# Kernel tuning notes

Measured on AMD Instinct MI355X. Metric: run time of the kernel, lower is better.

## Reference

```python
import jax, jax.numpy as jnp
import numpy as np

B, T, D, H = 1024, 200, 64, 64


def setup_inputs() -> dict:
    key = jax.random.key(0)
    ks = jax.random.split(key, 24)
    s = 0.05
    inp = {
        'dense_inputs': jax.random.normal(ks[0], (B, 4), jnp.float32),
        'sparse_inputs': jax.random.randint(ks[1], (B, 2), 0, 1000),
        'seq_inputs': jax.random.randint(ks[2], (B, T, 1), 0, 1000000),
        'item_inputs': jax.random.randint(ks[3], (B, 1), 0, 1000000),
        'hist_len': jax.random.randint(ks[4], (B,), 1, T + 1),
        'item_table': jax.random.normal(ks[5], (1000000, D), jnp.float32) * s,
        'other_tables': jax.random.normal(ks[6], (2, 1000, 16), jnp.float32) * s,
        'gru_W': jax.random.normal(ks[7], (D, 3 * H), jnp.float32) * s,
        'gru_U': jax.random.normal(ks[8], (H, 3 * H), jnp.float32) * s,
        'gru_b': jnp.zeros((3 * H,), jnp.float32),
        'aug_W': jax.random.normal(ks[9], (H, 3 * H), jnp.float32) * s,
        'aug_U': jax.random.normal(ks[10], (H, 3 * H), jnp.float32) * s,
        'aug_b': jnp.zeros((3 * H,), jnp.float32),
        'att_W1': jax.random.normal(ks[11], (4 * D, 64), jnp.float32) * s,
        'att_b1': jnp.zeros((64,), jnp.float32),
        'att_W2': jax.random.normal(ks[12], (64, 16), jnp.float32) * s,
        'att_b2': jnp.zeros((16,), jnp.float32),
        'att_W3': jax.random.normal(ks[13], (16, 1), jnp.float32) * s,
        'att_b3': jnp.zeros((1,), jnp.float32),
        'ffn_W1': jax.random.normal(ks[14], (164, 256), jnp.float32) * s,
        'ffn_b1': jnp.zeros((256,), jnp.float32),
        'ffn_W2': jax.random.normal(ks[15], (256, 128), jnp.float32) * s,
        'ffn_b2': jnp.zeros((128,), jnp.float32),
        'ffn_W3': jax.random.normal(ks[16], (128, 64), jnp.float32) * s,
        'ffn_b3': jnp.zeros((64,), jnp.float32),
        'out_W': jax.random.normal(ks[17], (64, 1), jnp.float32) * s,
        'out_b': jnp.zeros((1,), jnp.float32),
    }
    return inp


def _gru_scan(x_tbd, valid_tb, W, U, b, att_tb=None):
    """Masked (AU)GRU scan. x_tbd: [T,B,D]; valid_tb: [T,B] bool; att_tb: [T,B] or None.
    Returns (final_state [B,H], seq_states [T,B,H])."""
    h0 = jnp.zeros((x_tbd.shape[1], H), x_tbd.dtype)

    def step(h, inp):
        x, valid, a = inp
        xw = x @ W + b            # [B,3H]
        hu = h @ U                # [B,3H]
        z = jax.nn.sigmoid(xw[:, :H] + hu[:, :H])
        r = jax.nn.sigmoid(xw[:, H:2 * H] + hu[:, H:2 * H])
        hh = jnp.tanh(xw[:, 2 * H:] + r * hu[:, 2 * H:])
        if a is not None:
            z = a[:, None] * z    # AUGRU: attention-scaled update gate
        h_new = (1.0 - z) * h + z * hh
        h = jnp.where(valid[:, None], h_new, h)
        return h, h

    xs = (x_tbd, valid_tb, att_tb)
    if att_tb is None:
        def step2(h, inp):
            return step(h, (inp[0], inp[1], None))
        return jax.lax.scan(step2, h0, (x_tbd, valid_tb))
    return jax.lax.scan(step, h0, xs)


def _dice(x):
    # Dice activation at alpha=0: p=sigmoid(batch-standardized x); out = p*x
    m = jnp.mean(x, axis=0, keepdims=True)
    v = jnp.var(x, axis=0, keepdims=True)
    p = jax.nn.sigmoid((x - m) * jax.lax.rsqrt(v + 1e-9))
    return p * x


def reference(dense_inputs, sparse_inputs, seq_inputs, item_inputs, hist_len,
              item_table, other_tables, gru_W, gru_U, gru_b, aug_W, aug_U, aug_b,
              att_W1, att_b1, att_W2, att_b2, att_W3, att_b3,
              ffn_W1, ffn_b1, ffn_W2, ffn_b2, ffn_W3, ffn_b3, out_W, out_b):
    # Embedding lookups
    seq_embed = item_table[seq_inputs[:, :, 0]]          # [B,T,D]
    target_embed = item_table[item_inputs[:, 0]]         # [B,D]
    other = jnp.concatenate([other_tables[i][sparse_inputs[:, i]] for i in range(2)], axis=-1)  # [B,32]
    other_info = jnp.concatenate([dense_inputs, other], axis=-1)  # [B,36]

    valid_tb = jnp.arange(T)[:, None] < hist_len[None, :]  # [T,B]

    # Interest extraction: plain GRU over behavior sequence
    _, seq_h_tbh = _gru_scan(jnp.transpose(seq_embed, (1, 0, 2)), valid_tb, gru_W, gru_U, gru_b)
    seq_h = jnp.transpose(seq_h_tbh, (1, 0, 2))           # [B,T,H]

    # DIN-style target attention: MLP over [q, k, q-k, q*k]
    qt = jnp.broadcast_to(target_embed[:, None, :], seq_h.shape)
    feats = jnp.concatenate([qt, seq_h, qt - seq_h, qt * seq_h], axis=-1)  # [B,T,4D]
    prelu = lambda x: jnp.where(x > 0, x, 0.25 * x)
    a = prelu(feats @ att_W1 + att_b1)
    a = prelu(a @ att_W2 + att_b2)
    logits = (a @ att_W3 + att_b3)[..., 0]                # [B,T]
    logits = jnp.where(valid_tb.T, logits, -1e9)
    scores = jax.nn.softmax(logits, axis=-1)              # [B,T]

    # Interest evolution: AUGRU gated by attention scores
    final_state, _ = _gru_scan(seq_h_tbh, valid_tb, aug_W, aug_U, aug_b, att_tb=scores.T)

    out = jnp.concatenate([final_state, target_embed, other_info], axis=-1)  # [B,164]
    out = _dice(out @ ffn_W1 + ffn_b1)
    out = _dice(out @ ffn_W2 + ffn_b2)
    out = _dice(out @ ffn_W3 + ffn_b3)
    out = jax.nn.sigmoid(out @ out_W + out_b)             # [B,1]
    return out
```

## Files before the change

### kernel.cpp

```cpp
#include <hip/hip_runtime.h>

#define BB 1024
#define TT 200

typedef __attribute__((ext_vector_type(8))) short short8;
typedef __attribute__((ext_vector_type(4))) float f32x4;

__device__ __forceinline__ float sigmoidf_(float x) { return __fdividef(1.0f, 1.0f + __expf(-x)); }
__device__ __forceinline__ float tanh_fast(float x) {
    x = fminf(15.f, fmaxf(-15.f, x));
    float e = __expf(-2.f * x);
    return __fdividef(1.f - e, 1.f + e);
}
__device__ __forceinline__ float dicef_(float x, float m, float v) {
    return x * sigmoidf_((x - m) * rsqrtf(v + 1e-9f));
}
__device__ __forceinline__ unsigned short f2bf(float f) {
    unsigned u = __float_as_uint(f);
    unsigned r = u + 0x7fffu + ((u >> 16) & 1u);
    return (unsigned short)(r >> 16);
}
__device__ __forceinline__ float bf2f(unsigned short h) {
    return __uint_as_float(((unsigned)h) << 16);
}
__device__ __forceinline__ unsigned cvt_pk_bf16(float lo, float hi) {
    unsigned r;
    asm("v_cvt_pk_bf16_f32 %0, %1, %2" : "=v"(r) : "v"(lo), "v"(hi));
    return r;
}
union U8 { short8 s8; unsigned u[4]; };

__global__ void k_prep(const float* __restrict__ dense, const int* __restrict__ sparse,
                       const int* __restrict__ item_idx, const float* __restrict__ table,
                       const float* __restrict__ other_tables,
                       float* __restrict__ target, float* __restrict__ other) {
    int b = blockIdx.x, l = threadIdx.x;
    target[b * 64 + l] = table[(size_t)item_idx[b] * 64 + l];
    if (l < 4) other[b * 36 + l] = dense[b * 4 + l];
    else if (l < 20) other[b * 36 + l] = other_tables[(size_t)sparse[b * 2 + 0] * 16 + (l - 4)];
    else if (l < 36) other[b * 36 + l] = other_tables[1000 * 16 + (size_t)sparse[b * 2 + 1] * 16 + (l - 20)];
}

template <int GATHER>
__global__ __launch_bounds__(256, 1) void k_xw(
    const int* __restrict__ idx, const float* __restrict__ tablef,
    const unsigned short* __restrict__ Abf,
    const float* __restrict__ W, const float* __restrict__ bias,
    unsigned short* __restrict__ out, int Mtiles, int tilestride)
{
    const int l = threadIdx.x & 63;
    const int wv = threadIdx.x >> 6;
    const int lg = l >> 4;
    const int li = l & 15;

    short8 bfr[12][2];
    float bn[12];
#pragma unroll
    for (int nt = 0; nt < 12; ++nt) {
        bn[nt] = bias[nt * 16 + li];
#pragma unroll
        for (int c = 0; c < 2; ++c) {
#pragma unroll
            for (int j = 0; j < 8; ++j) {
                int k = c * 32 + lg * 8 + j;
                bfr[nt][c][j] = (short)f2bf(W[k * 192 + nt * 16 + li]);
            }
        }
    }

    for (int tile = blockIdx.x * 4 + wv; tile < Mtiles; tile += tilestride) {
        short8 a[2];
        if (GATHER) {
            long row = (long)tile * 16 + li;
            long id = idx[row];
            const float* tp = tablef + id * 64 + lg * 8;
#pragma unroll
            for (int c = 0; c < 2; ++c) {
                f32x4 v0 = *(const f32x4*)(tp + c * 32);
                f32x4 v1 = *(const f32x4*)(tp + c * 32 + 4);
#pragma unroll
                for (int j = 0; j < 4; ++j) {
                    a[c][j] = (short)f2bf(v0[j]);
                    a[c][4 + j] = (short)f2bf(v1[j]);
                }
            }
        } else {
            long row = (long)tile * 16 + li;
#pragma unroll
            for (int c = 0; c < 2; ++c)
                a[c] = *(const short8*)(Abf + row * 64 + c * 32 + lg * 8);
        }

        f32x4 acc[12];
#pragma unroll
        for (int nt = 0; nt < 12; ++nt) acc[nt] = (f32x4){0.f, 0.f, 0.f, 0.f};
#pragma unroll
        for (int c = 0; c < 2; ++c)
#pragma unroll
            for (int nt = 0; nt < 12; ++nt)
                acc[nt] = __builtin_amdgcn_mfma_f32_16x16x32_bf16(a[c], bfr[nt][c], acc[nt], 0, 0, 0);

#pragma unroll
        for (int nt = 0; nt < 12; ++nt)
#pragma unroll
            for (int j = 0; j < 4; ++j) {
                long row = (long)tile * 16 + lg * 4 + j;
                out[row * 192 + nt * 16 + li] = f2bf(acc[nt][j] + bn[nt]);
            }
    }
}

template <int AUG>
__global__ __launch_bounds__(256, 1) void k_scan2(
    const unsigned short* __restrict__ xw,
    const float* __restrict__ U,
    const int* __restrict__ hist_len,
    const float* __restrict__ scores,
    unsigned short* __restrict__ hout,
    float* __restrict__ hfinal)
{
    __shared__ float h_lds[4][64];
    const int w = threadIdx.x >> 6, l = threadIdx.x & 63;
    const int b = blockIdx.x * 4 + w;

    float Uz[64], Ur[64], Uh[64];
#pragma unroll
    for (int k = 0; k < 64; ++k) {
        Uz[k] = U[k * 192 + l];
        Ur[k] = U[k * 192 + 64 + l];
        Uh[k] = U[k * 192 + 128 + l];
    }
    const int mylen = hist_len[b];
    const unsigned short* xwr = xw + (size_t)b * TT * 192;
    const float* scr = scores + (size_t)b * TT;
    unsigned short* hor = hout + (size_t)b * TT * 64;

    float h = 0.f;
    h_lds[w][l] = 0.f;
    asm volatile("" ::: "memory");

    unsigned short nz = xwr[l], nr = xwr[64 + l], nh = xwr[128 + l];
    float ns = AUG ? scr[0] : 0.f;

    for (int t = 0; t < TT; ++t) {
        const unsigned short cz = nz, cr = nr, ch = nh;
        const float cs = ns;
        if (t + 1 < TT) {
            const unsigned short* p = xwr + (size_t)(t + 1) * 192;
            nz = p[l]; nr = p[64 + l]; nh = p[128 + l];
            if (AUG) ns = scr[t + 1];
        }

        float az = 0.f, ar = 0.f, ah = 0.f;
        const float4* h4 = (const float4*)(&h_lds[w][0]);
#pragma unroll
        for (int kc = 0; kc < 16; ++kc) {
            float4 hv = h4[kc];
            az += hv.x * Uz[4*kc] + hv.y * Uz[4*kc+1] + hv.z * Uz[4*kc+2] + hv.w * Uz[4*kc+3];
            ar += hv.x * Ur[4*kc] + hv.y * Ur[4*kc+1] + hv.z * Ur[4*kc+2] + hv.w * Ur[4*kc+3];
            ah += hv.x * Uh[4*kc] + hv.y * Uh[4*kc+1] + hv.z * Uh[4*kc+2] + hv.w * Uh[4*kc+3];
        }

        float zg = sigmoidf_(bf2f(cz) + az);
        float rg = sigmoidf_(bf2f(cr) + ar);
        float hh = tanh_fast(bf2f(ch) + rg * ah);
        if (AUG) zg *= cs;
        float hn = (1.f - zg) * h + zg * hh;
        h = (t < mylen) ? hn : h;

        asm volatile("" ::: "memory");
        h_lds[w][l] = h;
        asm volatile("" ::: "memory");
        if (!AUG) hor[(size_t)t * 64 + l] = f2bf(h);
    }
    if (AUG) hfinal[(size_t)b * 64 + l] = h;
}

__global__ __launch_bounds__(256, 2) void k_att(
    const float* __restrict__ target, const unsigned short* __restrict__ seq_hb,
    const float* __restrict__ W1, const float* __restrict__ b1,
    const float* __restrict__ W2, const float* __restrict__ b2,
    const float* __restrict__ W3, const float* __restrict__ b3,
    const int* __restrict__ hist_len, float* __restrict__ scores)
{
    __shared__ unsigned short W1f[8 * 4 * 64 * 8];
    __shared__ float a1s[4][16][68];
    __shared__ float logit_lds[208];
    __shared__ float red[8];

    const int tid = threadIdx.x;
    const int wv = tid >> 6, l = tid & 63;
    const int lg = l >> 4, li = l & 15;
    const int b = blockIdx.x;
    const int len = hist_len[b];

    for (int i = tid; i < 8 * 4 * 64 * 8; i += 256) {
        int j = i & 7, ll = (i >> 3) & 63, nt = (i >> 9) & 3, c = i >> 11;
        int k = c * 32 + (ll >> 4) * 8 + j;
        int col = nt * 16 + (ll & 15);
        W1f[i] = f2bf(W1[k * 64 + col]);
    }
    __syncthreads();

    short8 w1r[8][4];
    const short8* wf = (const short8*)W1f;
#pragma unroll
    for (int c = 0; c < 8; ++c)
#pragma unroll
        for (int nt = 0; nt < 4; ++nt)
            w1r[c][nt] = wf[(c * 4 + nt) * 64 + l];

    short8 w2r[2];
#pragma unroll
    for (int c = 0; c < 2; ++c) {
        U8 t8;
#pragma unroll
        for (int m = 0; m < 4; ++m) {
            int k0 = c * 32 + lg * 8 + 2 * m;
            t8.u[m] = cvt_pk_bf16(W2[k0 * 16 + li], W2[(k0 + 1) * 16 + li]);
        }
        w2r[c] = t8.s8;
    }

    float b1v[4];
#pragma unroll
    for (int nt = 0; nt < 4; ++nt) b1v[nt] = b1[nt * 16 + li];
    const float b2v = b2[li];
    const float w3v = W3[li];
    const float b3r = b3[0];

    const float* qp = target + (size_t)b * 64;
    float qf_lo[8], qf_hi[8];
#pragma unroll
    for (int j = 0; j < 8; ++j) { qf_lo[j] = qp[lg * 8 + j]; qf_hi[j] = qp[32 + lg * 8 + j]; }
    U8 q8l, q8h;
#pragma unroll
    for (int m = 0; m < 4; ++m) {
        q8l.u[m] = cvt_pk_bf16(qf_lo[2 * m], qf_lo[2 * m + 1]);
        q8h.u[m] = cvt_pk_bf16(qf_hi[2 * m], qf_hi[2 * m + 1]);
    }

    for (int mt = wv; mt < 13; mt += 4) {
        const int t = mt * 16 + li;
        const int tld = (t < TT) ? t : TT - 1;
        const unsigned short* hp = seq_hb + ((size_t)b * TT + tld) * 64 + lg * 8;
        short8 h8l = *(const short8*)hp;
        short8 h8h = *(const short8*)(hp + 32);

        float hf;
        U8 d8l, d8h, m8l, m8h;
#pragma unroll
        for (int m = 0; m < 4; ++m) {
            float h0, h1, d0, d1, p0, p1;
            h0 = bf2f((unsigned short)h8l[2 * m]); h1 = bf2f((unsigned short)h8l[2 * m + 1]);
            d0 = qf_lo[2 * m] - h0; d1 = qf_lo[2 * m + 1] - h1;
            p0 = qf_lo[2 * m] * h0; p1 = qf_lo[2 * m + 1] * h1;
            d8l.u[m] = cvt_pk_bf16(d0, d1);
            m8l.u[m] = cvt_pk_bf16(p0, p1);
            h0 = bf2f((unsigned short)h8h[2 * m]); h1 = bf2f((unsigned short)h8h[2 * m + 1]);
            d0 = qf_hi[2 * m] - h0; d1 = qf_hi[2 * m + 1] - h1;
            p0 = qf_hi[2 * m] * h0; p1 = qf_hi[2 * m + 1] * h1;
            d8h.u[m] = cvt_pk_bf16(d0, d1);
            m8h.u[m] = cvt_pk_bf16(p0, p1);
        }
        (void)hf;

        f32x4 acc[4];
#pragma unroll
        for (int nt = 0; nt < 4; ++nt) acc[nt] = (f32x4){0.f, 0.f, 0.f, 0.f};
#pragma unroll
        for (int nt = 0; nt < 4; ++nt) {
            acc[nt] = __builtin_amdgcn_mfma_f32_16x16x32_bf16(q8l.s8, w1r[0][nt], acc[nt], 0, 0, 0);
            acc[nt] = __builtin_amdgcn_mfma_f32_16x16x32_bf16(q8h.s8, w1r[1][nt], acc[nt], 0, 0, 0);
            acc[nt] = __builtin_amdgcn_mfma_f32_16x16x32_bf16(h8l,    w1r[2][nt], acc[nt], 0, 0, 0);
            acc[nt] = __builtin_amdgcn_mfma_f32_16x16x32_bf16(h8h,    w1r[3][nt], acc[nt], 0, 0, 0);
            acc[nt] = __builtin_amdgcn_mfma_f32_16x16x32_bf16(d8l.s8, w1r[4][nt], acc[nt], 0, 0, 0);
            acc[nt] = __builtin_amdgcn_mfma_f32_16x16x32_bf16(d8h.s8, w1r[5][nt], acc[nt], 0, 0, 0);
            acc[nt] = __builtin_amdgcn_mfma_f32_16x16x32_bf16(m8l.s8, w1r[6][nt], acc[nt], 0, 0, 0);
            acc[nt] = __builtin_amdgcn_mfma_f32_16x16x32_bf16(m8h.s8, w1r[7][nt], acc[nt], 0, 0, 0);
        }

#pragma unroll
        for (int nt = 0; nt < 4; ++nt)
#pragma unroll
            for (int jj = 0; jj < 4; ++jj) {
                float v = acc[nt][jj] + b1v[nt];
                a1s[wv][lg * 4 + jj][nt * 16 + li] = (v > 0.f) ? v : 0.25f * v;
            }

        const float* arow = &a1s[wv][li][0];
        f32x4 acc2 = (f32x4){0.f, 0.f, 0.f, 0.f};
#pragma unroll
        for (int c2 = 0; c2 < 2; ++c2) {
            f32x4 v0 = *(const f32x4*)(arow + c2 * 32 + lg * 8);
            f32x4 v1 = *(const f32x4*)(arow + c2 * 32 + lg * 8 + 4);
            U8 a2f;
            a2f.u[0] = cvt_pk_bf16(v0[0], v0[1]);
            a2f.u[1] = cvt_pk_bf16(v0[2], v0[3]);
            a2f.u[2] = cvt_pk_bf16(v1[0], v1[1]);
            a2f.u[3] = cvt_pk_bf16(v1[2], v1[3]);
            acc2 = __builtin_amdgcn_mfma_f32_16x16x32_bf16(a2f.s8, w2r[c2], acc2, 0, 0, 0);
        }

#pragma unroll
        for (int jj = 0; jj < 4; ++jj) {
            float a2 = acc2[jj] + b2v;
            a2 = (a2 > 0.f) ? a2 : 0.25f * a2;
            float part = a2 * w3v;
            part += __shfl_xor(part, 1);
            part += __shfl_xor(part, 2);
            part += __shfl_xor(part, 4);
            part += __shfl_xor(part, 8);
            int tt = mt * 16 + lg * 4 + jj;
            if (li == 0 && tt < TT)
                logit_lds[tt] = (tt < len) ? (part + b3r) : -1e9f;
        }
    }
    __syncthreads();

    float v = (tid < TT) ? logit_lds[tid] : -1e30f;
    float m = v;
#pragma unroll
    for (int s = 1; s < 64; s <<= 1) m = fmaxf(m, __shfl_xor(m, s));
    if (l == 0) red[wv] = m;
    __syncthreads();
    m = fmaxf(fmaxf(red[0], red[1]), fmaxf(red[2], red[3]));
    float e = (tid < TT) ? __expf(v - m) : 0.f;
    float sum = e;
#pragma unroll
    for (int s = 1; s < 64; s <<= 1) sum += __shfl_xor(sum, s);
    if (l == 0) red[4 + wv] = sum;
    __syncthreads();
    float inv = __fdividef(1.f, red[4] + red[5] + red[6] + red[7]);
    if (tid < TT) scores[(size_t)b * TT + tid] = e * inv;
}

__global__ __launch_bounds__(256) void k_fc1(const float* __restrict__ fin,
                                             const float* __restrict__ tgt,
                                             const float* __restrict__ oth,
                                             const float* __restrict__ Wt,
                                             const float* __restrict__ bvec,
                                             float* __restrict__ fout) {
    __shared__ float z0[164];
    int b = blockIdx.x, tid = threadIdx.x;
    if (tid < 64) z0[tid] = fin[b * 64 + tid];
    else if (tid < 128) z0[tid] = tgt[b * 64 + tid - 64];
    else if (tid < 164) z0[tid] = oth[b * 36 + tid - 128];
    __syncthreads();
    float acc = bvec[tid];
#pragma unroll 4
    for (int k = 0; k < 164; ++k) acc += z0[k] * Wt[k * 256 + tid];
    fout[(size_t)b * 256 + tid] = acc;
}

template <int F>
__global__ __launch_bounds__(256) void k_stats(const float* __restrict__ x, float* __restrict__ stat) {
    int c = blockIdx.x, tid = threadIdx.x;
    float s = 0.f, sq = 0.f;
    for (int i = tid; i < BB; i += 256) {
        float v = x[(size_t)i * F + c];
        s += v; sq += v * v;
    }
#pragma unroll
    for (int m = 1; m < 64; m <<= 1) { s += __shfl_xor(s, m); sq += __shfl_xor(sq, m); }
    __shared__ float rs[4], rq[4];
    if ((tid & 63) == 0) { rs[tid >> 6] = s; rq[tid >> 6] = sq; }
    __syncthreads();
    if (tid == 0) {
        float S = rs[0] + rs[1] + rs[2] + rs[3];
        float Q = rq[0] + rq[1] + rq[2] + rq[3];
        float mean = S * (1.f / BB);
        float var = Q * (1.f / BB) - mean * mean;
        stat[c] = mean;
        stat[F + c] = var;
    }
}

__global__ __launch_bounds__(256) void k_fc2(const float* __restrict__ f1,
                                             const float* __restrict__ st1,
                                             const float* __restrict__ Wt,
                                             const float* __restrict__ bvec,
                                             float* __restrict__ f2) {
    __shared__ float z[256];
    int b = blockIdx.x, tid = threadIdx.x;
    float x = f1[(size_t)b * 256 + tid];
    z[tid] = dicef_(x, st1[tid], st1[256 + tid]);
    __syncthreads();
    if (tid < 128) {
        float acc = bvec[tid];
#pragma unroll 4
        for (int k = 0; k < 256; ++k) acc += z[k] * Wt[k * 128 + tid];
        f2[(size_t)b * 128 + tid] = acc;
    }
}

__global__ __launch_bounds__(128) void k_fc3(const float* __restrict__ f2,
                                             const float* __restrict__ st2,
                                             const float* __restrict__ Wt,
                                             const float* __restrict__ bvec,
                                             float* __restrict__ f3) {
    __shared__ float z[128];
    int b = blockIdx.x, tid = threadIdx.x;
    float x = f2[(size_t)b * 128 + tid];
    z[tid] = dicef_(x, st2[tid], st2[128 + tid]);
    __syncthreads();
    if (tid < 64) {
        float acc = bvec[tid];
#pragma unroll 4
        for (int k = 0; k < 128; ++k) acc += z[k] * Wt[k * 64 + tid];
        f3[(size_t)b * 64 + tid] = acc;
    }
}

__global__ void k_out(const float* __restrict__ f3, const float* __restrict__ st3,
                      const float* __restrict__ outW, const float* __restrict__ outb,
                      float* __restrict__ out) {
    int b = blockIdx.x, l = threadIdx.x;
    float x = f3[(size_t)b * 64 + l];
    float z = dicef_(x, st3[l], st3[64 + l]);
    float p = z * outW[l];
#pragma unroll
    for (int m = 1; m < 64; m <<= 1) p += __shfl_xor(p, m);
    if (l == 0) out[b] = sigmoidf_(p + outb[0]);
}

extern "C" void kernel_launch(void* const* d_in, const int* in_sizes, int n_in,
                              void* d_out, int out_size, void* d_ws, size_t ws_size,
                              hipStream_t stream) {
    const float* dense      = (const float*)d_in[0];
    const int*   sparse     = (const int*)d_in[1];
    const int*   seq_idx    = (const int*)d_in[2];
    const int*   item_idx   = (const int*)d_in[3];
    const int*   hist_len   = (const int*)d_in[4];
    const float* item_table = (const float*)d_in[5];
    const float* other_tab  = (const float*)d_in[6];
    const float* gru_W = (const float*)d_in[7];
    const float* gru_U = (const float*)d_in[8];
    const float* gru_b = (const float*)d_in[9];
    const float* aug_W = (const float*)d_in[10];
    const float* aug_U = (const float*)d_in[11];
    const float* aug_b = (const float*)d_in[12];
    const float* att_W1 = (const float*)d_in[13];
    const float* att_b1 = (const float*)d_in[14];
    const float* att_W2 = (const float*)d_in[15];
    const float* att_b2 = (const float*)d_in[16];
    const float* att_W3 = (const float*)d_in[17];
    const float* att_b3 = (const float*)d_in[18];
    const float* ffn_W1 = (const float*)d_in[19];
    const float* ffn_b1 = (const float*)d_in[20];
    const float* ffn_W2 = (const float*)d_in[21];
    const float* ffn_b2 = (const float*)d_in[22];
    const float* ffn_W3 = (const float*)d_in[23];
    const float* ffn_b3 = (const float*)d_in[24];
    const float* out_W  = (const float*)d_in[25];
    const float* out_b  = (const float*)d_in[26];

    float* wsf = (float*)d_ws;
    unsigned short* xwb   = (unsigned short*)(wsf);
    unsigned short* seqhb = (unsigned short*)(wsf + 19660800);
    float* scores = wsf + 26214400;
    float* target = wsf + 26419200;
    float* other  = wsf + 26484736;
    float* finals = wsf + 26521600;
    float* f1     = wsf + 26587136;
    float* f2     = wsf + 26849280;
    float* f3     = wsf + 26980352;
    float* st1    = wsf + 27045888;
    float* st2    = wsf + 27046400;
    float* st3    = wsf + 27046656;

    float* dout = (float*)d_out;
    const int Mtiles = (BB * TT) / 16;

    k_prep<<<BB, 64, 0, stream>>>(dense, sparse, item_idx, item_table, other_tab, target, other);

    k_xw<1><<<800, 256, 0, stream>>>(seq_idx, item_table, nullptr, gru_W, gru_b, xwb, Mtiles, 3200);

    k_scan2<0><<<BB / 4, 256, 0, stream>>>(xwb, gru_U, hist_len, scores, seqhb, finals);

    k_att<<<BB, 256, 0, stream>>>(target, seqhb, att_W1, att_b1, att_W2, att_b2,
                                  att_W3, att_b3, hist_len, scores);

    k_xw<0><<<800, 256, 0, stream>>>(nullptr, nullptr, seqhb, aug_W, aug_b, xwb, Mtiles, 3200);

    k_scan2<1><<<BB / 4, 256, 0, stream>>>(xwb, aug_U, hist_len, scores, seqhb, finals);

    k_fc1<<<BB, 256, 0, stream>>>(finals, target, other, ffn_W1, ffn_b1, f1);
    k_stats<256><<<256, 256, 0, stream>>>(f1, st1);
    k_fc2<<<BB, 256, 0, stream>>>(f1, st1, ffn_W2, ffn_b2, f2);
    k_stats<128><<<128, 256, 0, stream>>>(f2, st2);
    k_fc3<<<BB, 128, 0, stream>>>(f2, st2, ffn_W3, ffn_b3, f3);
    k_stats<64><<<64, 256, 0, stream>>>(f3, st3);
    k_out<<<BB, 64, 0, stream>>>(f3, st3, out_W, out_b, dout);
}
```

Baseline: 479.7 us.

## Split GRU recurrence matvec across four waves per batch row with LDS reduction

The scan kernel now assigns one block per batch row instead of one wave per row, with each of four waves holding a 16-row slice of U. The waves compute partial gate dot products, reduce them through shared memory, and one wave, rotating by timestep, applies the gate nonlinearity and updates h. This cuts the serial per-step dot-product length and the register pressure, allowing higher occupancy and four times more blocks. In exchange it adds two block barriers and an LDS reduction on every timestep of the sequential chain.

```diff
diff --git a/kernel.cpp b/kernel.cpp
--- a/kernel.cpp
+++ b/kernel.cpp
@@ -111,7 +111,7 @@
 }
 
 template <int AUG>
-__global__ __launch_bounds__(256, 1) void k_scan2(
+__global__ __launch_bounds__(256, 4) void k_scan3(
     const unsigned short* __restrict__ xw,
     const float* __restrict__ U,
     const int* __restrict__ hist_len,
@@ -119,61 +119,74 @@
     unsigned short* __restrict__ hout,
     float* __restrict__ hfinal)
 {
-    __shared__ float h_lds[4][64];
-    const int w = threadIdx.x >> 6, l = threadIdx.x & 63;
-    const int b = blockIdx.x * 4 + w;
-
-    float Uz[64], Ur[64], Uh[64];
-#pragma unroll
-    for (int k = 0; k < 64; ++k) {
-        Uz[k] = U[k * 192 + l];
-        Ur[k] = U[k * 192 + 64 + l];
-        Uh[k] = U[k * 192 + 128 + l];
-    }
-    const int mylen = hist_len[b];
+    __shared__ float h_lds[64];
+    __shared__ float part[3][4][64];
+
+    const int tid = threadIdx.x;
+    const int w = tid >> 6, l = tid & 63;
+    const int b = blockIdx.x;
+
+    float Uz[16], Ur[16], Uh[16];
+#pragma unroll
+    for (int kk = 0; kk < 16; ++kk) {
+        int k = w * 16 + kk;
+        Uz[kk] = U[k * 192 + l];
+        Ur[kk] = U[k * 192 + 64 + l];
+        Uh[kk] = U[k * 192 + 128 + l];
+    }
     const unsigned short* xwr = xw + (size_t)b * TT * 192;
     const float* scr = scores + (size_t)b * TT;
     unsigned short* hor = hout + (size_t)b * TT * 64;
-
-    float h = 0.f;
-    h_lds[w][l] = 0.f;
-    asm volatile("" ::: "memory");
-
-    unsigned short nz = xwr[l], nr = xwr[64 + l], nh = xwr[128 + l];
-    float ns = AUG ? scr[0] : 0.f;
+    const int mylen = hist_len[b];
+
+    unsigned short nz = 0, nr_ = 0, nh = 0;
+    float ns = 0.f;
+    if (w == 0) {
+        nz = xwr[l]; nr_ = xwr[64 + l]; nh = xwr[128 + l];
+        if (AUG) ns = scr[0];
+        h_lds[l] = 0.f;
+    }
+    __syncthreads();
 
     for (int t = 0; t < TT; ++t) {
-        const unsigned short cz = nz, cr = nr, ch = nh;
-        const float cs = ns;
-        if (t + 1 < TT) {
+        if (t + 1 < TT && ((t + 1) & 3) == w) {
             const unsigned short* p = xwr + (size_t)(t + 1) * 192;
-            nz = p[l]; nr = p[64 + l]; nh = p[128 + l];
+            nz = p[l]; nr_ = p[64 + l]; nh = p[128 + l];
             if (AUG) ns = scr[t + 1];
         }
 
         float az = 0.f, ar = 0.f, ah = 0.f;
-        const float4* h4 = (const float4*)(&h_lds[w][0]);
-#pragma unroll
-        for (int kc = 0; kc < 16; ++kc) {
+        const float4* h4 = (const float4*)(&h_lds[w * 16]);
+#pragma unroll
+        for (int kc = 0; kc < 4; ++kc) {
             float4 hv = h4[kc];
             az += hv.x * Uz[4*kc] + hv.y * Uz[4*kc+1] + hv.z * Uz[4*kc+2] + hv.w * Uz[4*kc+3];
             ar += hv.x * Ur[4*kc] + hv.y * Ur[4*kc+1] + hv.z * Ur[4*kc+2] + hv.w * Ur[4*kc+3];
             ah += hv.x * Uh[4*kc] + hv.y * Uh[4*kc+1] + hv.z * Uh[4*kc+2] + hv.w * Uh[4*kc+3];
         }
-
-        float zg = sigmoidf_(bf2f(cz) + az);
-        float rg = sigmoidf_(bf2f(cr) + ar);
-        float hh = tanh_fast(bf2f(ch) + rg * ah);
-        if (AUG) zg *= cs;
-        float hn = (1.f - zg) * h + zg * hh;
-        h = (t < mylen) ? hn : h;
-
-        asm volatile("" ::: "memory");
-        h_lds[w][l] = h;
-        asm volatile("" ::: "memory");
-        if (!AUG) hor[(size_t)t * 64 + l] = f2bf(h);
-    }
-    if (AUG) hfinal[(size_t)b * 64 + l] = h;
+        part[0][w][l] = az;
+        part[1][w][l] = ar;
+        part[2][w][l] = ah;
+        __syncthreads();
+
+        if ((t & 3) == w) {
+            float azf = part[0][0][l] + part[0][1][l] + part[0][2][l] + part[0][3][l];
+            float arf = part[1][0][l] + part[1][1][l] + part[1][2][l] + part[1][3][l];
+            float ahf = part[2][0][l] + part[2][1][l] + part[2][2][l] + part[2][3][l];
+            float hprev = h_lds[l];
+
+            float zg = sigmoidf_(bf2f(nz) + azf);
+            float rg = sigmoidf_(bf2f(nr_) + arf);
+            float hh = tanh_fast(bf2f(nh) + rg * ahf);
+            if (AUG) zg *= ns;
+            float hn = (1.f - zg) * hprev + zg * hh;
+            float hval = (t < mylen) ? hn : hprev;
+            h_lds[l] = hval;
+            if (!AUG) hor[(size_t)t * 64 + l] = f2bf(hval);
+        }
+        __syncthreads();
+    }
+    if (AUG && w == 0) hfinal[(size_t)b * 64 + l] = h_lds[l];
 }
 
 __global__ __launch_bounds__(256, 2) void k_att(
@@ -247,7 +260,6 @@
         short8 h8l = *(const short8*)hp;
         short8 h8h = *(const short8*)(hp + 32);
 
-        float hf;
         U8 d8l, d8h, m8l, m8h;
 #pragma unroll
         for (int m = 0; m < 4; ++m) {
@@ -263,7 +275,6 @@
             d8h.u[m] = cvt_pk_bf16(d0, d1);
             m8h.u[m] = cvt_pk_bf16(p0, p1);
         }
-        (void)hf;
 
         f32x4 acc[4];
 #pragma unroll
@@ -476,14 +487,14 @@
 
     k_xw<1><<<800, 256, 0, stream>>>(seq_idx, item_table, nullptr, gru_W, gru_b, xwb, Mtiles, 3200);
 
-    k_scan2<0><<<BB / 4, 256, 0, stream>>>(xwb, gru_U, hist_len, scores, seqhb, finals);
+    k_scan3<0><<<BB, 256, 0, stream>>>(xwb, gru_U, hist_len, scores, seqhb, finals);
 
     k_att<<<BB, 256, 0, stream>>>(target, seqhb, att_W1, att_b1, att_W2, att_b2,
                                   att_W3, att_b3, hist_len, scores);
 
     k_xw<0><<<800, 256, 0, stream>>>(nullptr, nullptr, seqhb, aug_W, aug_b, xwb, Mtiles, 3200);
 
-    k_scan2<1><<<BB / 4, 256, 0, stream>>>(xwb, aug_U, hist_len, scores, seqhb, finals);
+    k_scan3<1><<<BB, 256, 0, stream>>>(xwb, aug_U, hist_len, scores, seqhb, finals);
 
     k_fc1<<<BB, 256, 0, stream>>>(finals, target, other, ffn_W1, ffn_b1, f1);
     k_stats<256><<<256, 256, 0, stream>>>(f1, st1);
```

Result: faster. 431.0 us (-10.1%).

## Batch 16 sequences per block in GRU scans and use bf16 MFMA recurrence

Applied to the files above, without the earlier changes.

The GRU/AUGRU recurrent kernel now handles 16 batch rows per 256-thread block instead of 4. The h@U product runs on bf16 MFMA 16x16x32 instructions, with U held as bf16 fragments and the hidden state stored as bf16 in a swizzled, double-buffered LDS tile that is synced once per step. Each wave computes a 16-column slice of the gates for all 16 rows. The aim is to replace the scalar fp32 FMA loop over 192 U registers per lane with matrix cores and to make each block do more work per step. The cost is 64 blocks instead of 256, leaving most of the GPU idle. It also adds a block-wide barrier every step and rounds the recurrent state and U to bf16, which loses precision.

```diff
diff --git a/kernel.cpp b/kernel.cpp
--- a/kernel.cpp
+++ b/kernel.cpp
@@ -111,7 +111,7 @@
 }
 
 template <int AUG>
-__global__ __launch_bounds__(256, 1) void k_scan2(
+__global__ __launch_bounds__(256, 1) void k_scan4(
     const unsigned short* __restrict__ xw,
     const float* __restrict__ U,
     const int* __restrict__ hist_len,
@@ -119,61 +119,121 @@
     unsigned short* __restrict__ hout,
     float* __restrict__ hfinal)
 {
-    __shared__ float h_lds[4][64];
-    const int w = threadIdx.x >> 6, l = threadIdx.x & 63;
-    const int b = blockIdx.x * 4 + w;
-
-    float Uz[64], Ur[64], Uh[64];
-#pragma unroll
-    for (int k = 0; k < 64; ++k) {
-        Uz[k] = U[k * 192 + l];
-        Ur[k] = U[k * 192 + 64 + l];
-        Uh[k] = U[k * 192 + 128 + l];
-    }
-    const int mylen = hist_len[b];
-    const unsigned short* xwr = xw + (size_t)b * TT * 192;
-    const float* scr = scores + (size_t)b * TT;
-    unsigned short* hor = hout + (size_t)b * TT * 64;
-
-    float h = 0.f;
-    h_lds[w][l] = 0.f;
-    asm volatile("" ::: "memory");
-
-    unsigned short nz = xwr[l], nr = xwr[64 + l], nh = xwr[128 + l];
-    float ns = AUG ? scr[0] : 0.f;
+    __shared__ unsigned short hbuf[2][16][64];
+
+    const int tid = threadIdx.x;
+    const int w = tid >> 6, l = tid & 63;
+    const int lg = l >> 4, li = l & 15;
+    const int row0 = blockIdx.x * 16;
+    const int myrow = row0 + li;
+    const int g0 = w * 16 + lg * 4;
+    const int sw = (li & 7) << 4;
+
+    short8 uzA[2], urA[2], uhA[2];
+#pragma unroll
+    for (int c = 0; c < 2; ++c) {
+#pragma unroll
+        for (int j = 0; j < 8; ++j) {
+            int k = c * 32 + lg * 8 + j;
+            uzA[c][j] = (short)f2bf(U[k * 192 + (16 * w + li)]);
+            urA[c][j] = (short)f2bf(U[k * 192 + 64 + (16 * w + li)]);
+            uhA[c][j] = (short)f2bf(U[k * 192 + 128 + (16 * w + li)]);
+        }
+    }
+
+    const unsigned short* xwrow = xw + (size_t)myrow * TT * 192;
+    const float* scrow = scores + (size_t)myrow * TT;
+    const int mylen = hist_len[myrow];
+
+    char* wb[2];
+    wb[0] = (char*)&hbuf[0][li][0] + ((w * 32 + lg * 8) ^ sw);
+    wb[1] = (char*)&hbuf[1][li][0] + ((w * 32 + lg * 8) ^ sw);
+    const char* rbase[2] = {(const char*)&hbuf[0][li][0], (const char*)&hbuf[1][li][0]};
+    const int ro0 = (lg * 16) ^ sw;
+    const int ro1 = (64 + lg * 16) ^ sw;
+
+    float hp0 = 0.f, hp1 = 0.f, hp2 = 0.f, hp3 = 0.f;
+    *(uint2*)wb[0] = (uint2){0u, 0u};
+
+    uint2 pz = *(const uint2*)(xwrow + g0);
+    uint2 pr = *(const uint2*)(xwrow + 64 + g0);
+    uint2 ph = *(const uint2*)(xwrow + 128 + g0);
+    float psc = AUG ? scrow[0] : 0.f;
+    __syncthreads();
 
     for (int t = 0; t < TT; ++t) {
-        const unsigned short cz = nz, cr = nr, ch = nh;
-        const float cs = ns;
+        const uint2 cz = pz, cr = pr, ch = ph;
+        const float cs = psc;
         if (t + 1 < TT) {
-            const unsigned short* p = xwr + (size_t)(t + 1) * 192;
-            nz = p[l]; nr = p[64 + l]; nh = p[128 + l];
-            if (AUG) ns = scr[t + 1];
-        }
-
-        float az = 0.f, ar = 0.f, ah = 0.f;
-        const float4* h4 = (const float4*)(&h_lds[w][0]);
-#pragma unroll
-        for (int kc = 0; kc < 16; ++kc) {
-            float4 hv = h4[kc];
-            az += hv.x * Uz[4*kc] + hv.y * Uz[4*kc+1] + hv.z * Uz[4*kc+2] + hv.w * Uz[4*kc+3];
-            ar += hv.x * Ur[4*kc] + hv.y * Ur[4*kc+1] + hv.z * Ur[4*kc+2] + hv.w * Ur[4*kc+3];
-            ah += hv.x * Uh[4*kc] + hv.y * Uh[4*kc+1] + hv.z * Uh[4*kc+2] + hv.w * Uh[4*kc+3];
-        }
-
-        float zg = sigmoidf_(bf2f(cz) + az);
-        float rg = sigmoidf_(bf2f(cr) + ar);
-        float hh = tanh_fast(bf2f(ch) + rg * ah);
-        if (AUG) zg *= cs;
-        float hn = (1.f - zg) * h + zg * hh;
-        h = (t < mylen) ? hn : h;
-
-        asm volatile("" ::: "memory");
-        h_lds[w][l] = h;
-        asm volatile("" ::: "memory");
-        if (!AUG) hor[(size_t)t * 64 + l] = f2bf(h);
-    }
-    if (AUG) hfinal[(size_t)b * 64 + l] = h;
+            const unsigned short* p = xwrow + (size_t)(t + 1) * 192;
+            pz = *(const uint2*)(p + g0);
+            pr = *(const uint2*)(p + 64 + g0);
+            ph = *(const uint2*)(p + 128 + g0);
+            if (AUG) psc = scrow[t + 1];
+        }
+
+        const char* rb = rbase[t & 1];
+        short8 b0 = *(const short8*)(rb + ro0);
+        short8 b1 = *(const short8*)(rb + ro1);
+
+        f32x4 az = (f32x4){0.f, 0.f, 0.f, 0.f};
+        f32x4 ar = (f32x4){0.f, 0.f, 0.f, 0.f};
+        f32x4 ah = (f32x4){0.f, 0.f, 0.f, 0.f};
+        az = __builtin_amdgcn_mfma_f32_16x16x32_bf16(uzA[0], b0, az, 0, 0, 0);
+        ar = __builtin_amdgcn_mfma_f32_16x16x32_bf16(urA[0], b0, ar, 0, 0, 0);
+        ah = __builtin_amdgcn_mfma_f32_16x16x32_bf16(uhA[0], b0, ah, 0, 0, 0);
+        az = __builtin_amdgcn_mfma_f32_16x16x32_bf16(uzA[1], b1, az, 0, 0, 0);
+        ar = __builtin_amdgcn_mfma_f32_16x16x32_bf16(urA[1], b1, ar, 0, 0, 0);
+        ah = __builtin_amdgcn_mfma_f32_16x16x32_bf16(uhA[1], b1, ah, 0, 0, 0);
+
+        float xz0 = __uint_as_float(cz.x << 16), xz1 = __uint_as_float(cz.x & 0xffff0000u);
+        float xz2 = __uint_as_float(cz.y << 16), xz3 = __uint_as_float(cz.y & 0xffff0000u);
+        float xr0 = __uint_as_float(cr.x << 16), xr1 = __uint_as_float(cr.x & 0xffff0000u);
+        float xr2 = __uint_as_float(cr.y << 16), xr3 = __uint_as_float(cr.y & 0xffff0000u);
+        float xh0 = __uint_as_float(ch.x << 16), xh1 = __uint_as_float(ch.x & 0xffff0000u);
+        float xh2 = __uint_as_float(ch.y << 16), xh3 = __uint_as_float(ch.y & 0xffff0000u);
+
+        const bool upd = (t < mylen);
+        {
+            float zg = sigmoidf_(xz0 + az[0]); if (AUG) zg *= cs;
+            float rg = sigmoidf_(xr0 + ar[0]);
+            float hv = tanh_fast(xh0 + rg * ah[0]);
+            float hn = (1.f - zg) * hp0 + zg * hv;
+            hp0 = upd ? hn : hp0;
+        }
+        {
+            float zg = sigmoidf_(xz1 + az[1]); if (AUG) zg *= cs;
+            float rg = sigmoidf_(xr1 + ar[1]);
+            float hv = tanh_fast(xh1 + rg * ah[1]);
+            float hn = (1.f - zg) * hp1 + zg * hv;
+            hp1 = upd ? hn : hp1;
+        }
+        {
+            float zg = sigmoidf_(xz2 + az[2]); if (AUG) zg *= cs;
+            float rg = sigmoidf_(xr2 + ar[2]);
+            float hv = tanh_fast(xh2 + rg * ah[2]);
+            float hn = (1.f - zg) * hp2 + zg * hv;
+            hp2 = upd ? hn : hp2;
+        }
+        {
+            float zg = sigmoidf_(xz3 + az[3]); if (AUG) zg *= cs;
+            float rg = sigmoidf_(xr3 + ar[3]);
+            float hv = tanh_fast(xh3 + rg * ah[3]);
+            float hn = (1.f - zg) * hp3 + zg * hv;
+            hp3 = upd ? hn : hp3;
+        }
+
+        const unsigned q0 = cvt_pk_bf16(hp0, hp1);
+        const unsigned q1 = cvt_pk_bf16(hp2, hp3);
+        *(uint2*)wb[(t + 1) & 1] = (uint2){q0, q1};
+        if (!AUG)
+            *(uint2*)(hout + ((size_t)myrow * TT + t) * 64 + g0) = (uint2){q0, q1};
+        __syncthreads();
+    }
+    if (AUG) {
+        f32x4 hv = (f32x4){hp0, hp1, hp2, hp3};
+        *(f32x4*)(hfinal + (size_t)myrow * 64 + g0) = hv;
+    }
 }
 
 __global__ __launch_bounds__(256, 2) void k_att(
@@ -247,7 +307,6 @@
         short8 h8l = *(const short8*)hp;
         short8 h8h = *(const short8*)(hp + 32);
 
-        float hf;
         U8 d8l, d8h, m8l, m8h;
 #pragma unroll
         for (int m = 0; m < 4; ++m) {
@@ -263,7 +322,6 @@
             d8h.u[m] = cvt_pk_bf16(d0, d1);
             m8h.u[m] = cvt_pk_bf16(p0, p1);
         }
-        (void)hf;
 
         f32x4 acc[4];
 #pragma unroll
@@ -476,14 +534,14 @@
 
     k_xw<1><<<800, 256, 0, stream>>>(seq_idx, item_table, nullptr, gru_W, gru_b, xwb, Mtiles, 3200);
 
-    k_scan2<0><<<BB / 4, 256, 0, stream>>>(xwb, gru_U, hist_len, scores, seqhb, finals);
+    k_scan4<0><<<BB / 16, 256, 0, stream>>>(xwb, gru_U, hist_len, scores, seqhb, finals);
 
     k_att<<<BB, 256, 0, stream>>>(target, seqhb, att_W1, att_b1, att_W2, att_b2,
                                   att_W3, att_b3, hist_len, scores);
 
     k_xw<0><<<800, 256, 0, stream>>>(nullptr, nullptr, seqhb, aug_W, aug_b, xwb, Mtiles, 3200);
 
-    k_scan2<1><<<BB / 4, 256, 0, stream>>>(xwb, aug_U, hist_len, scores, seqhb, finals);
+    k_scan4<1><<<BB / 16, 256, 0, stream>>>(xwb, aug_U, hist_len, scores, seqhb, finals);
 
     k_fc1<<<BB, 256, 0, stream>>>(finals, target, other, ffn_W1, ffn_b1, f1);
     k_stats<256><<<256, 256, 0, stream>>>(f1, st1);
```

Measured after the change: 640.5 us. +33.5%, slower.

## Skip padded timesteps in GRU scans, projections and attention; one-wave scan blocks

Applied to the files above, without the earlier changes.

The GRU scans now stop at each sequence's hist_len instead of running all 200 steps. The non-augmented scan back-fills the frozen state for the padded steps so that later consumers still see correct values. The projection kernel skips 16-row tiles whose rows are all past their sequence length, and attention skips fully padded tiles by pre-filling those logits with -1e9. The scan also moves to one 64-thread block per batch row, with the recurrent weights held as vector registers and accumulated with vector FMAs. The aim is to remove wasted compute on padding, which is about half the work with uniform lengths, at the cost of load imbalance across waves.

```diff
diff --git a/kernel.cpp b/kernel.cpp
--- a/kernel.cpp
+++ b/kernel.cpp
@@ -29,6 +29,8 @@
     return r;
 }
 union U8 { short8 s8; unsigned u[4]; };
+
+#define REP16(M) M(0) M(1) M(2) M(3) M(4) M(5) M(6) M(7) M(8) M(9) M(10) M(11) M(12) M(13) M(14) M(15)
 
 __global__ void k_prep(const float* __restrict__ dense, const int* __restrict__ sparse,
                        const int* __restrict__ item_idx, const float* __restrict__ table,
@@ -46,6 +48,7 @@
     const int* __restrict__ idx, const float* __restrict__ tablef,
     const unsigned short* __restrict__ Abf,
     const float* __restrict__ W, const float* __restrict__ bias,
+    const int* __restrict__ hist_len,
     unsigned short* __restrict__ out, int Mtiles, int tilestride)
 {
     const int l = threadIdx.x & 63;
@@ -69,9 +72,16 @@
     }
 
     for (int tile = blockIdx.x * 4 + wv; tile < Mtiles; tile += tilestride) {
+        long row = (long)tile * 16 + li;
+        {
+            int bb = (int)(row / TT);
+            int tt = (int)(row - (long)bb * TT);
+            int vld = (tt < hist_len[bb]) ? 1 : 0;
+            if (__ballot(vld) == 0ull) continue;
+        }
+
         short8 a[2];
         if (GATHER) {
-            long row = (long)tile * 16 + li;
             long id = idx[row];
             const float* tp = tablef + id * 64 + lg * 8;
 #pragma unroll
@@ -85,7 +95,6 @@
                 }
             }
         } else {
-            long row = (long)tile * 16 + li;
 #pragma unroll
             for (int c = 0; c < 2; ++c)
                 a[c] = *(const short8*)(Abf + row * 64 + c * 32 + lg * 8);
@@ -104,14 +113,21 @@
         for (int nt = 0; nt < 12; ++nt)
 #pragma unroll
             for (int j = 0; j < 4; ++j) {
-                long row = (long)tile * 16 + lg * 4 + j;
-                out[row * 192 + nt * 16 + li] = f2bf(acc[nt][j] + bn[nt]);
+                long orow = (long)tile * 16 + lg * 4 + j;
+                out[orow * 192 + nt * 16 + li] = f2bf(acc[nt][j] + bn[nt]);
             }
     }
 }
 
+#define DECL_U(i) f32x4 Uz##i, Ur##i, Uh##i;
+#define LOAD_U(i) \
+    Uz##i = (f32x4){U[(4*(i)+0)*192+l],     U[(4*(i)+1)*192+l],     U[(4*(i)+2)*192+l],     U[(4*(i)+3)*192+l]}; \
+    Ur##i = (f32x4){U[(4*(i)+0)*192+64+l],  U[(4*(i)+1)*192+64+l],  U[(4*(i)+2)*192+64+l],  U[(4*(i)+3)*192+64+l]}; \
+    Uh##i = (f32x4){U[(4*(i)+0)*192+128+l], U[(4*(i)+1)*192+128+l], U[(4*(i)+2)*192+128+l], U[(4*(i)+3)*192+128+l]};
+#define STEP_FMA(i) { f32x4 hh4 = HS4[i]; az4 += hh4 * Uz##i; ar4 += hh4 * Ur##i; ah4 += hh4 * Uh##i; }
+
 template <int AUG>
-__global__ __launch_bounds__(256, 1) void k_scan2(
+__global__ __launch_bounds__(64, 1) void k_scan5(
     const unsigned short* __restrict__ xw,
     const float* __restrict__ U,
     const int* __restrict__ hist_len,
@@ -119,61 +135,62 @@
     unsigned short* __restrict__ hout,
     float* __restrict__ hfinal)
 {
-    __shared__ float h_lds[4][64];
-    const int w = threadIdx.x >> 6, l = threadIdx.x & 63;
-    const int b = blockIdx.x * 4 + w;
-
-    float Uz[64], Ur[64], Uh[64];
-#pragma unroll
-    for (int k = 0; k < 64; ++k) {
-        Uz[k] = U[k * 192 + l];
-        Ur[k] = U[k * 192 + 64 + l];
-        Uh[k] = U[k * 192 + 128 + l];
-    }
-    const int mylen = hist_len[b];
+    __shared__ float hsh[64];
+    const int l = threadIdx.x;
+    const int b = blockIdx.x;
+    const int len = hist_len[b];
+
+    REP16(DECL_U)
+    REP16(LOAD_U)
+
     const unsigned short* xwr = xw + (size_t)b * TT * 192;
     const float* scr = scores + (size_t)b * TT;
     unsigned short* hor = hout + (size_t)b * TT * 64;
 
     float h = 0.f;
-    h_lds[w][l] = 0.f;
+    hsh[l] = 0.f;
     asm volatile("" ::: "memory");
 
     unsigned short nz = xwr[l], nr = xwr[64 + l], nh = xwr[128 + l];
     float ns = AUG ? scr[0] : 0.f;
 
-    for (int t = 0; t < TT; ++t) {
+    const f32x4* HS4 = (const f32x4*)hsh;
+
+    for (int t = 0; t < len; ++t) {
         const unsigned short cz = nz, cr = nr, ch = nh;
         const float cs = ns;
-        if (t + 1 < TT) {
+        if (t + 1 < len) {
             const unsigned short* p = xwr + (size_t)(t + 1) * 192;
             nz = p[l]; nr = p[64 + l]; nh = p[128 + l];
             if (AUG) ns = scr[t + 1];
         }
 
-        float az = 0.f, ar = 0.f, ah = 0.f;
-        const float4* h4 = (const float4*)(&h_lds[w][0]);
-#pragma unroll
-        for (int kc = 0; kc < 16; ++kc) {
-            float4 hv = h4[kc];
-            az += hv.x * Uz[4*kc] + hv.y * Uz[4*kc+1] + hv.z * Uz[4*kc+2] + hv.w * Uz[4*kc+3];
-            ar += hv.x * Ur[4*kc] + hv.y * Ur[4*kc+1] + hv.z * Ur[4*kc+2] + hv.w * Ur[4*kc+3];
-            ah += hv.x * Uh[4*kc] + hv.y * Uh[4*kc+1] + hv.z * Uh[4*kc+2] + hv.w * Uh[4*kc+3];
-        }
-
-        float zg = sigmoidf_(bf2f(cz) + az);
-        float rg = sigmoidf_(bf2f(cr) + ar);
-        float hh = tanh_fast(bf2f(ch) + rg * ah);
+        f32x4 az4 = (f32x4){0.f, 0.f, 0.f, 0.f};
+        f32x4 ar4 = (f32x4){0.f, 0.f, 0.f, 0.f};
+        f32x4 ah4 = (f32x4){0.f, 0.f, 0.f, 0.f};
+        REP16(STEP_FMA)
+        float azf = (az4[0] + az4[1]) + (az4[2] + az4[3]);
+        float arf = (ar4[0] + ar4[1]) + (ar4[2] + ar4[3]);
+        float ahf = (ah4[0] + ah4[1]) + (ah4[2] + ah4[3]);
+
+        float zg = sigmoidf_(bf2f(cz) + azf);
         if (AUG) zg *= cs;
-        float hn = (1.f - zg) * h + zg * hh;
-        h = (t < mylen) ? hn : h;
+        float rg = sigmoidf_(bf2f(cr) + arf);
+        float hv = tanh_fast(bf2f(ch) + rg * ahf);
+        h = (1.f - zg) * h + zg * hv;
 
         asm volatile("" ::: "memory");
-        h_lds[w][l] = h;
+        hsh[l] = h;
         asm volatile("" ::: "memory");
         if (!AUG) hor[(size_t)t * 64 + l] = f2bf(h);
     }
-    if (AUG) hfinal[(size_t)b * 64 + l] = h;
+
+    if (AUG) {
+        hfinal[(size_t)b * 64 + l] = h;
+    } else {
+        const unsigned short fro = f2bf(h);
+        for (int t = len; t < TT; ++t) hor[(size_t)t * 64 + l] = fro;
+    }
 }
 
 __global__ __launch_bounds__(256, 2) void k_att(
@@ -194,6 +211,7 @@
     const int b = blockIdx.x;
     const int len = hist_len[b];
 
+    if (tid < 208) logit_lds[tid] = -1e9f;
     for (int i = tid; i < 8 * 4 * 64 * 8; i += 256) {
         int j = i & 7, ll = (i >> 3) & 63, nt = (i >> 9) & 3, c = i >> 11;
         int k = c * 32 + (ll >> 4) * 8 + j;
@@ -240,14 +258,13 @@
         q8h.u[m] = cvt_pk_bf16(qf_hi[2 * m], qf_hi[2 * m + 1]);
     }
 
-    for (int mt = wv; mt < 13; mt += 4) {
+    for (int mt = wv; mt * 16 < len; mt += 4) {
         const int t = mt * 16 + li;
         const int tld = (t < TT) ? t : TT - 1;
         const unsigned short* hp = seq_hb + ((size_t)b * TT + tld) * 64 + lg * 8;
         short8 h8l = *(const short8*)hp;
         short8 h8h = *(const short8*)(hp + 32);
 
-        float hf;
         U8 d8l, d8h, m8l, m8h;
 #pragma unroll
         for (int m = 0; m < 4; ++m) {
@@ -263,7 +280,6 @@
             d8h.u[m] = cvt_pk_bf16(d0, d1);
             m8h.u[m] = cvt_pk_bf16(p0, p1);
         }
-        (void)hf;
 
         f32x4 acc[4];
 #pragma unroll
@@ -474,16 +490,16 @@
 
     k_prep<<<BB, 64, 0, stream>>>(dense, sparse, item_idx, item_table, other_tab, target, other);
 
-    k_xw<1><<<800, 256, 0, stream>>>(seq_idx, item_table, nullptr, gru_W, gru_b, xwb, Mtiles, 3200);
-
-    k_scan2<0><<<BB / 4, 256, 0, stream>>>(xwb, gru_U, hist_len, scores, seqhb, finals);
+    k_xw<1><<<800, 256, 0, stream>>>(seq_idx, item_table, nullptr, gru_W, gru_b, hist_len, xwb, Mtiles, 3200);
+
+    k_scan5<0><<<BB, 64, 0, stream>>>(xwb, gru_U, hist_len, scores, seqhb, finals);
 
     k_att<<<BB, 256, 0, stream>>>(target, seqhb, att_W1, att_b1, att_W2, att_b2,
                                   att_W3, att_b3, hist_len, scores);
 
-    k_xw<0><<<800, 256, 0, stream>>>(nullptr, nullptr, seqhb, aug_W, aug_b, xwb, Mtiles, 3200);
-
-    k_scan2<1><<<BB / 4, 256, 0, stream>>>(xwb, aug_U, hist_len, scores, seqhb, finals);
+    k_xw<0><<<800, 256, 0, stream>>>(nullptr, nullptr, seqhb, aug_W, aug_b, hist_len, xwb, Mtiles, 3200);
+
+    k_scan5<1><<<BB, 64, 0, stream>>>(xwb, aug_U, hist_len, scores, seqhb, finals);
 
     k_fc1<<<BB, 256, 0, stream>>>(finals, target, other, ffn_W1, ffn_b1, f1);
     k_stats<256><<<256, 256, 0, stream>>>(f1, st1);
```

New measurement: 477.0 us. No clear change (-0.6%).
